# Optimization experiments

Measured on AMD Instinct MI355X. Metric: run time of the kernel, lower is better.

The kernel has to match this reference:

```python
import jax, jax.numpy as jnp
import numpy as np

N = 50000   # nodes
E = 400000  # edges
IN = 32     # in_channel
M = 64      # mid_channel
L = 3       # num_layers
EPS = 1e-5


def layer_norm(x, g, b):
    mu = jnp.mean(x, axis=-1, keepdims=True)
    var = jnp.mean((x - mu) ** 2, axis=-1, keepdims=True)
    return (x - mu) / jnp.sqrt(var + EPS) * g + b


def setup_inputs() -> dict:
    key = jax.random.key(0)
    ks = jax.random.split(key, 14)
    s = 0.05
    return {
        "x": jax.random.normal(ks[0], (N, IN), jnp.float32),
        "edge_index": jax.random.randint(ks[1], (2, E), 0, N, jnp.int64),
        # node encoder: Linear(IN->M) + LayerNorm(M)
        "enc_W": jax.random.normal(ks[2], (IN, M), jnp.float32) * s,
        "enc_b": jnp.zeros((M,), jnp.float32),
        "enc_g": jnp.ones((M,), jnp.float32),
        "enc_beta": jnp.zeros((M,), jnp.float32),
        # per-layer pre-norm
        "ln_g": jnp.ones((L, M), jnp.float32),
        "ln_b": jnp.zeros((L, M), jnp.float32),
        # SAGEConvV2 edge MLP: Linear(2M->2M) -> ReLU -> Linear(2M->M)
        "W1": jax.random.normal(ks[3], (L, 2 * M, 2 * M), jnp.float32) * s,
        "b1": jnp.zeros((L, 2 * M), jnp.float32),
        "W2": jax.random.normal(ks[4], (L, 2 * M, M), jnp.float32) * s,
        "b2": jnp.zeros((L, M), jnp.float32),
        # root weight lin_r: Linear(M->M, bias=False)
        "Wr": jax.random.normal(ks[5], (L, M, M), jnp.float32) * s,
    }


def reference(x, edge_index, enc_W, enc_b, enc_g, enc_beta,
              ln_g, ln_b, W1, b1, W2, b2, Wr):
    src = edge_index[0]  # x_j source nodes
    dst = edge_index[1]  # x_i target nodes (aggregation index)
    # node encoder
    x = layer_norm(x @ enc_W + enc_b, enc_g, enc_beta)
    # mean-aggregation denominator (in-degree, clamped to 1 like PyG scatter-mean)
    deg = jax.ops.segment_sum(jnp.ones((E,), x.dtype), dst, num_segments=N)
    deg = jnp.maximum(deg, 1.0)[:, None]
    for l in range(L):  # small fixed layer count
        # res+ block: norm -> act -> (dropout: identity in eval) -> conv -> residual
        h = jax.nn.relu(layer_norm(x, ln_g[l], ln_b[l]))
        # message: concat([x_i, x_j]) -> 2-layer MLP   [E, 2M] -> [E, M]
        msg = jnp.concatenate([h[dst], h[src]], axis=-1)
        msg = jax.nn.relu(msg @ W1[l] + b1[l]) @ W2[l] + b2[l]
        # scatter-mean aggregate at target nodes
        agg = jax.ops.segment_sum(msg, dst, num_segments=N) / deg
        # root weight
        h = agg + h @ Wr[l]
        x = x + h
    return x
```

## Files before the change

### kernel.cpp

```cpp
#include <hip/hip_runtime.h>
#include <hip/hip_bf16.h>

#define N_NODES 50000
#define N_EDGES 400000
#define IN_CH 32
#define EPS 1e-5f
#define SCAN_NB ((N_NODES + 1023) / 1024)
#define EL_CAP 384

typedef __attribute__((ext_vector_type(8))) short bh8;
typedef __attribute__((ext_vector_type(4))) float fx4;
typedef __attribute__((ext_vector_type(2))) float fx2;

static __device__ __forceinline__ unsigned int f2bf(float f) {
    __hip_bfloat16 h = __float2bfloat16(f);
    return (unsigned int)*(unsigned short*)&h;
}
static __device__ __forceinline__ unsigned short f2bfu(float f) {
    __hip_bfloat16 h = __float2bfloat16(f);
    return *(unsigned short*)&h;
}
static __device__ __forceinline__ float bflo(unsigned int u) { return __uint_as_float(u << 16); }
static __device__ __forceinline__ float bfhi(unsigned int u) { return __uint_as_float(u & 0xffff0000u); }

__global__ void hist_kernel(const int* __restrict__ ei, int* __restrict__ cnt) {
    int e = blockIdx.x * 256 + threadIdx.x;
    if (e < N_EDGES) atomicAdd(&cnt[ei[N_EDGES + e]], 1);
}

__global__ __launch_bounds__(1024) void scan1_kernel(const int* __restrict__ cnt,
                                                     int* __restrict__ exw,
                                                     int* __restrict__ bsum) {
    int b = blockIdx.x, t = threadIdx.x;
    int i = b * 1024 + t;
    int v = (i < N_NODES) ? cnt[i] : 0;
    int lane = t & 63, w = t >> 6;
    int s = v;
    #pragma unroll
    for (int off = 1; off < 64; off <<= 1) {
        int u = __shfl_up(s, off, 64);
        if (lane >= off) s += u;
    }
    __shared__ int ws[16];
    if (lane == 63) ws[w] = s;
    __syncthreads();
    if (t < 16) {
        int sv = ws[t];
        #pragma unroll
        for (int off = 1; off < 16; off <<= 1) {
            int u = __shfl_up(sv, off, 64);
            if (lane >= off) sv += u;
        }
        ws[t] = sv;
    }
    __syncthreads();
    int prefix = (w > 0) ? ws[w - 1] : 0;
    int incl = s + prefix;
    if (i < N_NODES) exw[i] = incl - v;
    if (t == 1023) bsum[b] = incl;
}

__global__ __launch_bounds__(1024) void scan3_kernel(const int* __restrict__ exw,
                                                     const int* __restrict__ bsum,
                                                     int* __restrict__ rp,
                                                     int* __restrict__ cnt) {
    __shared__ int pfx;
    __shared__ int total;
    int b = blockIdx.x, t = threadIdx.x;
    if (t < 64) {
        int v = (t < SCAN_NB) ? bsum[t] : 0;
        #pragma unroll
        for (int off = 1; off < 64; off <<= 1) {
            int u = __shfl_up(v, off, 64);
            if (t >= off) v += u;
        }
        if (b == 0 && t == 0) pfx = 0;
        if (b > 0 && t == b - 1) pfx = v;
        if (t == SCAN_NB - 1) total = v;
    }
    __syncthreads();
    int i = b * 1024 + t;
    if (i < N_NODES) {
        rp[i] = exw[i] + pfx;
        cnt[i] = 0;
    }
    if (b == 0 && t == 0) rp[N_NODES] = total;
}

__global__ void fill_kernel(const int* __restrict__ ei, const int* __restrict__ rp,
                            int* __restrict__ cur, int* __restrict__ el) {
    int e = blockIdx.x * 256 + threadIdx.x;
    if (e < N_EDGES) {
        int d = ei[N_EDGES + e];
        int p = atomicAdd(&cur[d], 1);
        el[rp[d] + p] = ei[e];
    }
}

#define WCT_TOT (3 * 320 * 64)
#define W2T_TOT (3 * 64 * 128)
__global__ void repack_kernel(const float* __restrict__ W1, const float* __restrict__ Wr,
                              const float* __restrict__ W2,
                              unsigned short* __restrict__ WcT,
                              unsigned short* __restrict__ W2T) {
    int t = blockIdx.x * 256 + threadIdx.x;
    if (t < WCT_TOT) {
        int l = t / (320 * 64);
        int rem = t % (320 * 64);
        int j = rem / 64, c = rem % 64;
        float v;
        if (j < 128)      v = W1[(l * 128 + c) * 128 + j];
        else if (j < 256) v = W1[(l * 128 + 64 + c) * 128 + (j - 128)];
        else              v = Wr[(l * 64 + c) * 64 + (j - 256)];
        WcT[t] = f2bfu(v);
    } else if (t < WCT_TOT + W2T_TOT) {
        int t2 = t - WCT_TOT;
        int l = t2 / 8192, rem = t2 % 8192;
        int n = rem / 128, k = rem % 128;
        W2T[t2] = f2bfu(W2[l * 8192 + k * 64 + n]);
    }
}

__global__ __launch_bounds__(256) void encoder_kernel(
    const float* __restrict__ x, const float* __restrict__ W,
    const float* __restrict__ b, const float* __restrict__ g,
    const float* __restrict__ beta, float* __restrict__ out) {
    __shared__ float wlds[IN_CH * 64];
    for (int t = threadIdx.x; t < IN_CH * 64; t += 256) wlds[t] = W[t];
    __syncthreads();
    int lane = threadIdx.x & 63;
    int node = blockIdx.x * 4 + (threadIdx.x >> 6);
    if (node >= N_NODES) return;
    float xv = (lane < IN_CH) ? x[node * IN_CH + lane] : 0.f;
    float acc = b[lane];
    #pragma unroll
    for (int c = 0; c < IN_CH; ++c) {
        float xc = __shfl(xv, c, 64);
        acc += xc * wlds[c * 64 + lane];
    }
    float s = acc;
    for (int off = 32; off; off >>= 1) s += __shfl_xor(s, off, 64);
    float mu = s * (1.f / 64.f);
    float d = acc - mu;
    float q = d * d;
    for (int off = 32; off; off >>= 1) q += __shfl_xor(q, off, 64);
    float r = rsqrtf(q * (1.f / 64.f) + EPS);
    out[node * 64 + lane] = d * r * g[lane] + beta[lane];
}

__global__ __launch_bounds__(256, 8) void fused7_kernel(
    float* __restrict__ x,
    const unsigned int* __restrict__ AbfI, const unsigned char* __restrict__ B8I,
    const unsigned short* __restrict__ W2T, const float* __restrict__ b2,
    const int* __restrict__ rp, const int* __restrict__ el,
    const float* __restrict__ g, const float* __restrict__ bvec,
    const unsigned short* __restrict__ WcT, const float* __restrict__ b1,
    unsigned short* __restrict__ AbfO, unsigned char* __restrict__ B8O,
    unsigned short* __restrict__ Rbf, int mode) {
    __shared__ float bufF[1088];
    __shared__ unsigned int slds[16][68];
    __shared__ int el_lds[EL_CAP];
    __shared__ int rp_lds[17];
    int tid = threadIdx.x;
    int lane = tid & 63, wid = tid >> 6;
    int l15 = lane & 15, g4 = lane >> 4;
    int base = blockIdx.x * 16;
    unsigned int* hU = (unsigned int*)bufF;
    int n = tid >> 4, sq = tid & 15;

    int col = wid * 16 + l15;
    int nd_l = base + g4 * 4;

    if (mode != 0) {
        if (tid < 17) rp_lds[tid] = rp[min(base + tid, N_NODES)];
        __syncthreads();
        int e0 = rp_lds[0];
        int nE = rp_lds[16] - e0;
        bool inl = (nE <= EL_CAP);
        if (inl) for (int t = tid; t < nE; t += 256) el_lds[t] = el[e0 + t];

        int nd_g = base + n;
        float av[8], acc[8];
        #pragma unroll
        for (int i = 0; i < 8; ++i) { av[i] = 0.f; acc[i] = 0.f; }
        {
            uint4 a0 = *(const uint4*)(AbfI + (size_t)min(nd_g, N_NODES - 1) * 64 + sq * 4);
            unsigned int aw[4] = {a0.x, a0.y, a0.z, a0.w};
            #pragma unroll
            for (int q = 0; q < 4; ++q) { av[2 * q] = bflo(aw[q]); av[2 * q + 1] = bfhi(aw[q]); }
        }
        __syncthreads();

        int es = rp_lds[n] - e0, ee = rp_lds[n + 1] - e0;
        int e2 = es;
        int cn = ee - e2; if (cn > 8) cn = 8;
        uint2 bufv[8];
        #pragma unroll
        for (int j = 0; j < 8; ++j)
            if (j < cn) {
                int src = inl ? el_lds[e2 + j] : el[e0 + e2 + j];
                bufv[j] = *(const uint2*)(B8I + (size_t)src * 128 + sq * 8);
            }
        while (cn > 0) {
            #pragma unroll
            for (int j = 0; j < 8; ++j)
                if (j < cn) {
                    fx2 f0 = __builtin_amdgcn_cvt_pk_f32_fp8((int)bufv[j].x, false);
                    fx2 f1 = __builtin_amdgcn_cvt_pk_f32_fp8((int)bufv[j].x, true);
                    fx2 f2 = __builtin_amdgcn_cvt_pk_f32_fp8((int)bufv[j].y, false);
                    fx2 f3 = __builtin_amdgcn_cvt_pk_f32_fp8((int)bufv[j].y, true);
                    acc[0] += fmaxf(av[0] + f0.x, 0.f);
                    acc[1] += fmaxf(av[1] + f0.y, 0.f);
                    acc[2] += fmaxf(av[2] + f1.x, 0.f);
                    acc[3] += fmaxf(av[3] + f1.y, 0.f);
                    acc[4] += fmaxf(av[4] + f2.x, 0.f);
                    acc[5] += fmaxf(av[5] + f2.y, 0.f);
                    acc[6] += fmaxf(av[6] + f3.x, 0.f);
                    acc[7] += fmaxf(av[7] + f3.y, 0.f);
                }
            e2 += cn;
            cn = ee - e2; if (cn > 8) cn = 8;
            #pragma unroll
            for (int j = 0; j < 8; ++j)
                if (j < cn) {
                    int src = inl ? el_lds[e2 + j] : el[e0 + e2 + j];
                    bufv[j] = *(const uint2*)(B8I + (size_t)src * 128 + sq * 8);
                }
        }
        #pragma unroll
        for (int jj = 0; jj < 4; ++jj)
            slds[n][sq * 4 + jj] = f2bf(acc[2 * jj]) | (f2bf(acc[2 * jj + 1]) << 16);

        float xpre[4], rpre[4];
        #pragma unroll
        for (int r = 0; r < 4; ++r) {
            int nd = min(nd_l + r, N_NODES - 1);
            xpre[r] = x[(size_t)nd * 64 + col];
            rpre[r] = bflo((unsigned int)Rbf[(size_t)nd * 64 + col]);
        }
        __syncthreads();

        bh8 sa[4];
        #pragma unroll
        for (int ks = 0; ks < 4; ++ks)
            sa[ks] = *(const bh8*)&slds[l15][ks * 16 + g4 * 4];
        fx4 accm = (fx4){0.f, 0.f, 0.f, 0.f};
        #pragma unroll
        for (int ks = 0; ks < 4; ++ks) {
            bh8 bf = *(const bh8*)(W2T + ((size_t)(wid * 16 + l15) * 128 + ks * 32 + g4 * 8));
            accm = __builtin_amdgcn_mfma_f32_16x16x32_bf16(sa[ks], bf, accm, 0, 0, 0);
        }
        float b2c = b2[col];
        #pragma unroll
        for (int r = 0; r < 4; ++r) {
            int lcl = g4 * 4 + r;
            int cv = rp_lds[lcl + 1] - rp_lds[lcl];
            float inv = cv > 0 ? 1.f / (float)cv : 0.f;
            float msk = cv > 0 ? 1.f : 0.f;
            int nd = nd_l + r;
            float xn = xpre[r] + accm[r] * inv + b2c * msk + rpre[r];
            if (nd < N_NODES) x[(size_t)nd * 64 + col] = xn;
            if (mode == 1) bufF[lcl * 68 + col] = xn;
        }
        if (mode == 2) return;
        __syncthreads();
    }

    {
        float vv[4];
        if (mode == 0) {
            int nd = base + n;
            float4 v0 = make_float4(0.f, 0.f, 0.f, 0.f);
            if (nd < N_NODES) v0 = ((const float4*)(x + (size_t)nd * 64))[sq];
            vv[0] = v0.x; vv[1] = v0.y; vv[2] = v0.z; vv[3] = v0.w;
        } else {
            #pragma unroll
            for (int i = 0; i < 4; ++i) vv[i] = bufF[n * 68 + sq * 4 + i];
        }
        float s = vv[0] + vv[1] + vv[2] + vv[3];
        s += __shfl_xor(s, 1, 16);
        s += __shfl_xor(s, 2, 16);
        s += __shfl_xor(s, 4, 16);
        s += __shfl_xor(s, 8, 16);
        float mu = s * (1.f / 64.f);
        float q = 0.f;
        #pragma unroll
        for (int i = 0; i < 4; ++i) { float d = vv[i] - mu; q += d * d; }
        q += __shfl_xor(q, 1, 16);
        q += __shfl_xor(q, 2, 16);
        q += __shfl_xor(q, 4, 16);
        q += __shfl_xor(q, 8, 16);
        float rs = rsqrtf(q * (1.f / 64.f) + EPS);
        float4 gg = *(const float4*)&g[sq * 4];
        float4 bb = *(const float4*)&bvec[sq * 4];
        float gv[4] = {gg.x, gg.y, gg.z, gg.w};
        float bv[4] = {bb.x, bb.y, bb.z, bb.w};
        __syncthreads();
        #pragma unroll
        for (int jj = 0; jj < 2; ++jj) {
            float h0 = fmaxf((vv[2 * jj] - mu) * rs * gv[2 * jj] + bv[2 * jj], 0.f);
            float h1 = fmaxf((vv[2 * jj + 1] - mu) * rs * gv[2 * jj + 1] + bv[2 * jj + 1], 0.f);
            hU[n * 33 + sq * 2 + jj] = f2bf(h0) | (f2bf(h1) << 16);
        }
    }
    __syncthreads();

    bh8 a2[2];
    #pragma unroll
    for (int ks = 0; ks < 2; ++ks)
        a2[ks] = *(const bh8*)&hU[l15 * 33 + ks * 16 + g4 * 4];
    int ndg = base + g4 * 4;
    #pragma unroll
    for (int nn = 0; nn < 5; ++nn) {
        int nb = wid * 5 + nn;
        fx4 c = (fx4){0.f, 0.f, 0.f, 0.f};
        #pragma unroll
        for (int ks = 0; ks < 2; ++ks) {
            bh8 bf = *(const bh8*)(WcT + ((size_t)(nb * 16 + l15) * 64 + ks * 32 + g4 * 8));
            c = __builtin_amdgcn_mfma_f32_16x16x32_bf16(a2[ks], bf, c, 0, 0, 0);
        }
        int colw = nb * 16 + l15;
        #pragma unroll
        for (int r = 0; r < 4; ++r) {
            int nd = ndg + r;
            if (nd >= N_NODES) continue;
            float v = c[r];
            if (colw < 128) {
                ((unsigned short*)AbfO)[(size_t)nd * 128 + colw] = f2bfu(v + b1[colw]);
            } else if (colw < 256) {
                unsigned int p = __builtin_amdgcn_cvt_pk_fp8_f32(v, v, 0, false);
                B8O[(size_t)nd * 128 + (colw - 128)] = (unsigned char)(p & 0xFF);
            } else {
                Rbf[(size_t)nd * 64 + (colw - 256)] = f2bfu(v);
            }
        }
    }
}

extern "C" void kernel_launch(void* const* d_in, const int* in_sizes, int n_in,
                              void* d_out, int out_size, void* d_ws, size_t ws_size,
                              hipStream_t stream) {
    const float* x       = (const float*)d_in[0];
    const int*   ei      = (const int*)d_in[1];
    const float* encW    = (const float*)d_in[2];
    const float* encb    = (const float*)d_in[3];
    const float* encg    = (const float*)d_in[4];
    const float* encbeta = (const float*)d_in[5];
    const float* lng     = (const float*)d_in[6];
    const float* lnb     = (const float*)d_in[7];
    const float* W1      = (const float*)d_in[8];
    const float* b1      = (const float*)d_in[9];
    const float* W2      = (const float*)d_in[10];
    const float* b2      = (const float*)d_in[11];
    const float* Wr      = (const float*)d_in[12];
    float* xout = (float*)d_out;

    char* ws = (char*)d_ws;
    size_t off = 0;
    auto alloc = [&](size_t bytes) -> void* {
        void* p = ws + off;
        off += (bytes + 255) & ~(size_t)255;
        return p;
    };
    unsigned short* WcT  = (unsigned short*)alloc(3 * 320 * 64 * sizeof(unsigned short));
    unsigned short* W2T  = (unsigned short*)alloc(3 * 64 * 128 * sizeof(unsigned short));
    unsigned int*   Abf0 = (unsigned int*)alloc((size_t)N_NODES * 128 * sizeof(unsigned short));
    unsigned int*   Abf1 = (unsigned int*)alloc((size_t)N_NODES * 128 * sizeof(unsigned short));
    unsigned char*  B80  = (unsigned char*)alloc((size_t)N_NODES * 128);
    unsigned char*  B81  = (unsigned char*)alloc((size_t)N_NODES * 128);
    unsigned short* Rbf  = (unsigned short*)alloc((size_t)N_NODES * 64 * sizeof(unsigned short));
    int*            cnt  = (int*)alloc(N_NODES * sizeof(int));
    int*            rp   = (int*)alloc((N_NODES + 1) * sizeof(int));
    int*            el   = (int*)alloc(N_EDGES * sizeof(int));
    int*            exw  = (int*)alloc(N_NODES * sizeof(int));
    int*            bsum = (int*)alloc(SCAN_NB * sizeof(int));

    hipMemsetAsync(cnt, 0, N_NODES * sizeof(int), stream);
    hist_kernel<<<(N_EDGES + 255) / 256, 256, 0, stream>>>(ei, cnt);
    scan1_kernel<<<SCAN_NB, 1024, 0, stream>>>(cnt, exw, bsum);
    scan3_kernel<<<SCAN_NB, 1024, 0, stream>>>(exw, bsum, rp, cnt);
    fill_kernel<<<(N_EDGES + 255) / 256, 256, 0, stream>>>(ei, rp, cnt, el);
    repack_kernel<<<(WCT_TOT + W2T_TOT + 255) / 256, 256, 0, stream>>>(W1, Wr, W2, WcT, W2T);

    encoder_kernel<<<(N_NODES + 3) / 4, 256, 0, stream>>>(x, encW, encb, encg, encbeta, xout);

    int gblocks = (N_NODES + 15) / 16;
    fused7_kernel<<<gblocks, 256, 0, stream>>>(
        xout, Abf0, B80, W2T, b2, rp, el, lng, lnb,
        WcT, b1, (unsigned short*)Abf0, B80, Rbf, 0);
    fused7_kernel<<<gblocks, 256, 0, stream>>>(
        xout, Abf0, B80, W2T, b2, rp, el, lng + 64, lnb + 64,
        WcT + (size_t)1 * 320 * 64, b1 + 128, (unsigned short*)Abf1, B81, Rbf, 1);
    fused7_kernel<<<gblocks, 256, 0, stream>>>(
        xout, Abf1, B81, W2T + (size_t)1 * 64 * 128, b2 + 64, rp, el, lng + 128, lnb + 128,
        WcT + (size_t)2 * 320 * 64, b1 + 256, (unsigned short*)Abf0, B80, Rbf, 1);
    fused7_kernel<<<gblocks, 256, 0, stream>>>(
        xout, Abf0, B80, W2T + (size_t)2 * 64 * 128, b2 + 128, rp, el, lng, lnb,
        WcT, b1, (unsigned short*)Abf1, B81, Rbf, 2);
}
```

Baseline: 229.2 us.

## Merge setup kernels, store destination-side projections in FP8, hoist residual loads

Folds the histogram, weight repack and node encoder into one launch using block-range dispatch, which removes two kernel launches. The per-node destination-side projection buffer (A) is now stored as FP8 instead of BF16, halving its footprint and the bytes read per node. The x and root-term loads are moved ahead of the edge aggregation loop so their latency can overlap it. The cost is lower precision in the A term and more register pressure from the earlier loads.

```diff
diff --git a/kernel.cpp b/kernel.cpp
--- a/kernel.cpp
+++ b/kernel.cpp
@@ -8,6 +8,12 @@
 #define SCAN_NB ((N_NODES + 1023) / 1024)
 #define EL_CAP 384
 
+#define HIST_B ((N_EDGES + 255) / 256)
+#define WCT_TOT (3 * 320 * 64)
+#define W2T_TOT (3 * 64 * 128)
+#define RPK_B ((WCT_TOT + W2T_TOT + 255) / 256)
+#define ENC_B ((N_NODES + 3) / 4)
+
 typedef __attribute__((ext_vector_type(8))) short bh8;
 typedef __attribute__((ext_vector_type(4))) float fx4;
 typedef __attribute__((ext_vector_type(2))) float fx2;
@@ -21,11 +27,63 @@
     return *(unsigned short*)&h;
 }
 static __device__ __forceinline__ float bflo(unsigned int u) { return __uint_as_float(u << 16); }
-static __device__ __forceinline__ float bfhi(unsigned int u) { return __uint_as_float(u & 0xffff0000u); }
-
-__global__ void hist_kernel(const int* __restrict__ ei, int* __restrict__ cnt) {
-    int e = blockIdx.x * 256 + threadIdx.x;
-    if (e < N_EDGES) atomicAdd(&cnt[ei[N_EDGES + e]], 1);
+
+__global__ __launch_bounds__(256) void setup_kernel(
+    const int* __restrict__ ei, int* __restrict__ cnt,
+    const float* __restrict__ W1, const float* __restrict__ Wr,
+    const float* __restrict__ W2,
+    unsigned short* __restrict__ WcT, unsigned short* __restrict__ W2T,
+    const float* __restrict__ x, const float* __restrict__ encW,
+    const float* __restrict__ encb, const float* __restrict__ encg,
+    const float* __restrict__ encbeta, float* __restrict__ xout) {
+    int b = blockIdx.x;
+    if (b < HIST_B) {
+        int e = b * 256 + threadIdx.x;
+        if (e < N_EDGES) atomicAdd(&cnt[ei[N_EDGES + e]], 1);
+        return;
+    }
+    b -= HIST_B;
+    if (b < RPK_B) {
+        int t = b * 256 + threadIdx.x;
+        if (t < WCT_TOT) {
+            int l = t / (320 * 64);
+            int rem = t % (320 * 64);
+            int j = rem / 64, c = rem % 64;
+            float v;
+            if (j < 128)      v = W1[(l * 128 + c) * 128 + j];
+            else if (j < 256) v = W1[(l * 128 + 64 + c) * 128 + (j - 128)];
+            else              v = Wr[(l * 64 + c) * 64 + (j - 256)];
+            WcT[t] = f2bfu(v);
+        } else if (t < WCT_TOT + W2T_TOT) {
+            int t2 = t - WCT_TOT;
+            int l = t2 / 8192, rem = t2 % 8192;
+            int n = rem / 128, k = rem % 128;
+            W2T[t2] = f2bfu(W2[l * 8192 + k * 64 + n]);
+        }
+        return;
+    }
+    b -= RPK_B;
+    __shared__ float wlds[IN_CH * 64];
+    for (int t = threadIdx.x; t < IN_CH * 64; t += 256) wlds[t] = encW[t];
+    __syncthreads();
+    int lane = threadIdx.x & 63;
+    int node = b * 4 + (threadIdx.x >> 6);
+    if (node >= N_NODES) return;
+    float xv = (lane < IN_CH) ? x[node * IN_CH + lane] : 0.f;
+    float acc = encb[lane];
+    #pragma unroll
+    for (int c = 0; c < IN_CH; ++c) {
+        float xc = __shfl(xv, c, 64);
+        acc += xc * wlds[c * 64 + lane];
+    }
+    float s = acc;
+    for (int off = 32; off; off >>= 1) s += __shfl_xor(s, off, 64);
+    float mu = s * (1.f / 64.f);
+    float d = acc - mu;
+    float q = d * d;
+    for (int off = 32; off; off >>= 1) q += __shfl_xor(q, off, 64);
+    float r = rsqrtf(q * (1.f / 64.f) + EPS);
+    xout[node * 64 + lane] = d * r * encg[lane] + encbeta[lane];
 }
 
 __global__ __launch_bounds__(1024) void scan1_kernel(const int* __restrict__ cnt,
@@ -97,65 +155,14 @@
     }
 }
 
-#define WCT_TOT (3 * 320 * 64)
-#define W2T_TOT (3 * 64 * 128)
-__global__ void repack_kernel(const float* __restrict__ W1, const float* __restrict__ Wr,
-                              const float* __restrict__ W2,
-                              unsigned short* __restrict__ WcT,
-                              unsigned short* __restrict__ W2T) {
-    int t = blockIdx.x * 256 + threadIdx.x;
-    if (t < WCT_TOT) {
-        int l = t / (320 * 64);
-        int rem = t % (320 * 64);
-        int j = rem / 64, c = rem % 64;
-        float v;
-        if (j < 128)      v = W1[(l * 128 + c) * 128 + j];
-        else if (j < 256) v = W1[(l * 128 + 64 + c) * 128 + (j - 128)];
-        else              v = Wr[(l * 64 + c) * 64 + (j - 256)];
-        WcT[t] = f2bfu(v);
-    } else if (t < WCT_TOT + W2T_TOT) {
-        int t2 = t - WCT_TOT;
-        int l = t2 / 8192, rem = t2 % 8192;
-        int n = rem / 128, k = rem % 128;
-        W2T[t2] = f2bfu(W2[l * 8192 + k * 64 + n]);
-    }
-}
-
-__global__ __launch_bounds__(256) void encoder_kernel(
-    const float* __restrict__ x, const float* __restrict__ W,
-    const float* __restrict__ b, const float* __restrict__ g,
-    const float* __restrict__ beta, float* __restrict__ out) {
-    __shared__ float wlds[IN_CH * 64];
-    for (int t = threadIdx.x; t < IN_CH * 64; t += 256) wlds[t] = W[t];
-    __syncthreads();
-    int lane = threadIdx.x & 63;
-    int node = blockIdx.x * 4 + (threadIdx.x >> 6);
-    if (node >= N_NODES) return;
-    float xv = (lane < IN_CH) ? x[node * IN_CH + lane] : 0.f;
-    float acc = b[lane];
-    #pragma unroll
-    for (int c = 0; c < IN_CH; ++c) {
-        float xc = __shfl(xv, c, 64);
-        acc += xc * wlds[c * 64 + lane];
-    }
-    float s = acc;
-    for (int off = 32; off; off >>= 1) s += __shfl_xor(s, off, 64);
-    float mu = s * (1.f / 64.f);
-    float d = acc - mu;
-    float q = d * d;
-    for (int off = 32; off; off >>= 1) q += __shfl_xor(q, off, 64);
-    float r = rsqrtf(q * (1.f / 64.f) + EPS);
-    out[node * 64 + lane] = d * r * g[lane] + beta[lane];
-}
-
-__global__ __launch_bounds__(256, 8) void fused7_kernel(
+__global__ __launch_bounds__(256, 8) void fused8_kernel(
     float* __restrict__ x,
-    const unsigned int* __restrict__ AbfI, const unsigned char* __restrict__ B8I,
+    const unsigned char* __restrict__ A8I, const unsigned char* __restrict__ B8I,
     const unsigned short* __restrict__ W2T, const float* __restrict__ b2,
     const int* __restrict__ rp, const int* __restrict__ el,
     const float* __restrict__ g, const float* __restrict__ bvec,
     const unsigned short* __restrict__ WcT, const float* __restrict__ b1,
-    unsigned short* __restrict__ AbfO, unsigned char* __restrict__ B8O,
+    unsigned char* __restrict__ A8O, unsigned char* __restrict__ B8O,
     unsigned short* __restrict__ Rbf, int mode) {
     __shared__ float bufF[1088];
     __shared__ unsigned int slds[16][68];
@@ -181,13 +188,24 @@
 
         int nd_g = base + n;
         float av[8], acc[8];
-        #pragma unroll
-        for (int i = 0; i < 8; ++i) { av[i] = 0.f; acc[i] = 0.f; }
         {
-            uint4 a0 = *(const uint4*)(AbfI + (size_t)min(nd_g, N_NODES - 1) * 64 + sq * 4);
-            unsigned int aw[4] = {a0.x, a0.y, a0.z, a0.w};
-            #pragma unroll
-            for (int q = 0; q < 4; ++q) { av[2 * q] = bflo(aw[q]); av[2 * q + 1] = bfhi(aw[q]); }
+            uint2 a0 = *(const uint2*)(A8I + (size_t)min(nd_g, N_NODES - 1) * 128 + sq * 8);
+            fx2 d0 = __builtin_amdgcn_cvt_pk_f32_fp8((int)a0.x, false);
+            fx2 d1 = __builtin_amdgcn_cvt_pk_f32_fp8((int)a0.x, true);
+            fx2 d2 = __builtin_amdgcn_cvt_pk_f32_fp8((int)a0.y, false);
+            fx2 d3 = __builtin_amdgcn_cvt_pk_f32_fp8((int)a0.y, true);
+            av[0] = d0.x; av[1] = d0.y; av[2] = d1.x; av[3] = d1.y;
+            av[4] = d2.x; av[5] = d2.y; av[6] = d3.x; av[7] = d3.y;
+        }
+        #pragma unroll
+        for (int i = 0; i < 8; ++i) acc[i] = 0.f;
+
+        float xpre[4], rpre[4];
+        #pragma unroll
+        for (int r = 0; r < 4; ++r) {
+            int nd = min(nd_l + r, N_NODES - 1);
+            xpre[r] = x[(size_t)nd * 64 + col];
+            rpre[r] = bflo((unsigned int)Rbf[(size_t)nd * 64 + col]);
         }
         __syncthreads();
 
@@ -230,14 +248,6 @@
         #pragma unroll
         for (int jj = 0; jj < 4; ++jj)
             slds[n][sq * 4 + jj] = f2bf(acc[2 * jj]) | (f2bf(acc[2 * jj + 1]) << 16);
-
-        float xpre[4], rpre[4];
-        #pragma unroll
-        for (int r = 0; r < 4; ++r) {
-            int nd = min(nd_l + r, N_NODES - 1);
-            xpre[r] = x[(size_t)nd * 64 + col];
-            rpre[r] = bflo((unsigned int)Rbf[(size_t)nd * 64 + col]);
-        }
         __syncthreads();
 
         bh8 sa[4];
@@ -326,9 +336,10 @@
             if (nd >= N_NODES) continue;
             float v = c[r];
             if (colw < 128) {
-                ((unsigned short*)AbfO)[(size_t)nd * 128 + colw] = f2bfu(v + b1[colw]);
+                unsigned int p = __builtin_amdgcn_cvt_pk_fp8_f32(v + b1[colw], 0.f, 0, false);
+                A8O[(size_t)nd * 128 + colw] = (unsigned char)(p & 0xFF);
             } else if (colw < 256) {
-                unsigned int p = __builtin_amdgcn_cvt_pk_fp8_f32(v, v, 0, false);
+                unsigned int p = __builtin_amdgcn_cvt_pk_fp8_f32(v, 0.f, 0, false);
                 B8O[(size_t)nd * 128 + (colw - 128)] = (unsigned char)(p & 0xFF);
             } else {
                 Rbf[(size_t)nd * 64 + (colw - 256)] = f2bfu(v);
@@ -364,8 +375,8 @@
     };
     unsigned short* WcT  = (unsigned short*)alloc(3 * 320 * 64 * sizeof(unsigned short));
     unsigned short* W2T  = (unsigned short*)alloc(3 * 64 * 128 * sizeof(unsigned short));
-    unsigned int*   Abf0 = (unsigned int*)alloc((size_t)N_NODES * 128 * sizeof(unsigned short));
-    unsigned int*   Abf1 = (unsigned int*)alloc((size_t)N_NODES * 128 * sizeof(unsigned short));
+    unsigned char*  A80  = (unsigned char*)alloc((size_t)N_NODES * 128);
+    unsigned char*  A81  = (unsigned char*)alloc((size_t)N_NODES * 128);
     unsigned char*  B80  = (unsigned char*)alloc((size_t)N_NODES * 128);
     unsigned char*  B81  = (unsigned char*)alloc((size_t)N_NODES * 128);
     unsigned short* Rbf  = (unsigned short*)alloc((size_t)N_NODES * 64 * sizeof(unsigned short));
@@ -376,25 +387,23 @@
     int*            bsum = (int*)alloc(SCAN_NB * sizeof(int));
 
     hipMemsetAsync(cnt, 0, N_NODES * sizeof(int), stream);
-    hist_kernel<<<(N_EDGES + 255) / 256, 256, 0, stream>>>(ei, cnt);
+    setup_kernel<<<HIST_B + RPK_B + ENC_B, 256, 0, stream>>>(
+        ei, cnt, W1, Wr, W2, WcT, W2T, x, encW, encb, encg, encbeta, xout);
     scan1_kernel<<<SCAN_NB, 1024, 0, stream>>>(cnt, exw, bsum);
     scan3_kernel<<<SCAN_NB, 1024, 0, stream>>>(exw, bsum, rp, cnt);
     fill_kernel<<<(N_EDGES + 255) / 256, 256, 0, stream>>>(ei, rp, cnt, el);
-    repack_kernel<<<(WCT_TOT + W2T_TOT + 255) / 256, 256, 0, stream>>>(W1, Wr, W2, WcT, W2T);
-
-    encoder_kernel<<<(N_NODES + 3) / 4, 256, 0, stream>>>(x, encW, encb, encg, encbeta, xout);
 
     int gblocks = (N_NODES + 15) / 16;
-    fused7_kernel<<<gblocks, 256, 0, stream>>>(
-        xout, Abf0, B80, W2T, b2, rp, el, lng, lnb,
-        WcT, b1, (unsigned short*)Abf0, B80, Rbf, 0);
-    fused7_kernel<<<gblocks, 256, 0, stream>>>(
-        xout, Abf0, B80, W2T, b2, rp, el, lng + 64, lnb + 64,
-        WcT + (size_t)1 * 320 * 64, b1 + 128, (unsigned short*)Abf1, B81, Rbf, 1);
-    fused7_kernel<<<gblocks, 256, 0, stream>>>(
-        xout, Abf1, B81, W2T + (size_t)1 * 64 * 128, b2 + 64, rp, el, lng + 128, lnb + 128,
-        WcT + (size_t)2 * 320 * 64, b1 + 256, (unsigned short*)Abf0, B80, Rbf, 1);
-    fused7_kernel<<<gblocks, 256, 0, stream>>>(
-        xout, Abf0, B80, W2T + (size_t)2 * 64 * 128, b2 + 128, rp, el, lng, lnb,
-        WcT, b1, (unsigned short*)Abf1, B81, Rbf, 2);
-}
+    fused8_kernel<<<gblocks, 256, 0, stream>>>(
+        xout, A80, B80, W2T, b2, rp, el, lng, lnb,
+        WcT, b1, A80, B80, Rbf, 0);
+    fused8_kernel<<<gblocks, 256, 0, stream>>>(
+        xout, A80, B80, W2T, b2, rp, el, lng + 64, lnb + 64,
+        WcT + (size_t)1 * 320 * 64, b1 + 128, A81, B81, Rbf, 1);
+    fused8_kernel<<<gblocks, 256, 0, stream>>>(
+        xout, A81, B81, W2T + (size_t)1 * 64 * 128, b2 + 64, rp, el, lng + 128, lnb + 128,
+        WcT + (size_t)2 * 320 * 64, b1 + 256, A80, B80, Rbf, 1);
+    fused8_kernel<<<gblocks, 256, 0, stream>>>(
+        xout, A80, B80, W2T + (size_t)2 * 64 * 128, b2 + 128, rp, el, lng, lnb,
+        WcT, b1, A81, B81, Rbf, 2);
+}
```

Result: no change. 229.5 us (+0.2%).
